# Optimization experiments

Measured on AMD Instinct MI355X. Metric: run time of the kernel, lower is better.

## Reference

```python
import jax, jax.numpy as jnp
import numpy as np

B, S, H, NH = 4, 1024, 768, 12
HD = H // NH  # head dim = 64


def setup_inputs() -> dict:
    key = jax.random.key(0)
    ks = jax.random.split(key, 8)
    scale = 0.02
    return {
        "hidden_states": jax.random.normal(ks[0], (B, S, H), jnp.float32),
        "attention_mask": jax.random.randint(ks[1], (B, 1, 1, S), 0, 2, jnp.int32),
        "rel_pos": jax.random.normal(ks[2], (B, NH, S, S), jnp.float32),
        "rel_2d_pos": jax.random.normal(ks[3], (B, NH, S, S), jnp.float32),
        "Wq": jax.random.normal(ks[4], (H, H), jnp.float32) * scale,
        "bq": jnp.zeros((H,), jnp.float32),
        "Wk": jax.random.normal(ks[5], (H, H), jnp.float32) * scale,
        "bk": jnp.zeros((H,), jnp.float32),
        "Wv": jax.random.normal(ks[6], (H, H), jnp.float32) * scale,
        "bv": jnp.zeros((H,), jnp.float32),
    }


def _heads(x):
    # [B,S,H] -> [B,NH,S,HD]
    return x.reshape(B, S, NH, HD).transpose(0, 2, 1, 3)


def reference(hidden_states, attention_mask, rel_pos, rel_2d_pos, Wq, bq, Wk, bk, Wv, bv):
    q = _heads(hidden_states @ Wq.T + bq) / jnp.sqrt(jnp.asarray(HD, hidden_states.dtype))
    k = _heads(hidden_states @ Wk.T + bk)
    v = _heads(hidden_states @ Wv.T + bv)
    # [B,NH,S,S] scores with additive relative 1D and 2D spatial biases
    scores = jnp.einsum("bhqd,bhkd->bhqk", q, k) + rel_pos + rel_2d_pos
    neg_min = jnp.finfo(jnp.float32).min
    scores = jnp.where(attention_mask.astype(bool), neg_min, scores.astype(jnp.float32))
    probs = jax.nn.softmax(scores, axis=-1).astype(v.dtype)  # dropout p applied only in training
    ctx = jnp.einsum("bhqk,bhkd->bhqd", probs, v)
    return ctx.transpose(0, 2, 1, 3).reshape(B, S, H)
```

## Files before the change

### kernel.cpp

```cpp
#include <hip/hip_runtime.h>
#include <hip/hip_bf16.h>
#include <cstdint>
#include <cstddef>

#define NB 4
#define SEQ 1024
#define HID 768
#define NHEAD 12
#define HD 64

typedef __bf16 bf16x8 __attribute__((ext_vector_type(8)));
typedef float f32x4 __attribute__((ext_vector_type(4)));

__device__ __forceinline__ unsigned short f2bf(float f) {
    unsigned int u = __float_as_uint(f);
    u += 0x7FFFu + ((u >> 16) & 1u);
    return (unsigned short)(u >> 16);
}

__global__ __launch_bounds__(256)
void qkv_kernel(const float* __restrict__ X,
                const float* __restrict__ Wq, const float* __restrict__ bq,
                const float* __restrict__ Wk, const float* __restrict__ bk,
                const float* __restrict__ Wv, const float* __restrict__ bv,
                unsigned short* __restrict__ qws,
                unsigned short* __restrict__ kws,
                unsigned short* __restrict__ vtws)
{
    __shared__ __align__(16) unsigned short Al[128 * 64];
    __shared__ __align__(16) unsigned short Bl[128 * 64];

    const int z = blockIdx.z;
    const float* Wp = (z == 0) ? Wq : ((z == 1) ? Wk : Wv);
    const float* bp = (z == 0) ? bq : ((z == 1) ? bk : bv);
    const int m0 = blockIdx.x * 128;
    const int n0 = blockIdx.y * 128;
    const int t = threadIdx.x;
    const int lane = t & 63;
    const int w = t >> 6;
    const int wm = w >> 1, wn = w & 1;
    const int l15 = lane & 15, l4 = lane >> 4;

    const f32x4 fzero = {0.f, 0.f, 0.f, 0.f};
    f32x4 acc[4][4];
#pragma unroll
    for (int a = 0; a < 4; ++a)
#pragma unroll
        for (int c = 0; c < 4; ++c) acc[a][c] = fzero;

    for (int k0 = 0; k0 < HID; k0 += 64) {
        __syncthreads();
#pragma unroll
        for (int i = 0; i < 8; ++i) {
            int idx = t + 256 * i;
            int row = idx >> 4;
            int c4  = idx & 15;
            float4 va = *(const float4*)(X + (size_t)(m0 + row) * HID + k0 + c4 * 4);
            ushort4 ua = make_ushort4(f2bf(va.x), f2bf(va.y), f2bf(va.z), f2bf(va.w));
            *(ushort4*)(Al + row * 64 + c4 * 4) = ua;
            float4 vb = *(const float4*)(Wp + (size_t)(n0 + row) * HID + k0 + c4 * 4);
            ushort4 ub = make_ushort4(f2bf(vb.x), f2bf(vb.y), f2bf(vb.z), f2bf(vb.w));
            *(ushort4*)(Bl + row * 64 + c4 * 4) = ub;
        }
        __syncthreads();
#pragma unroll
        for (int kc = 0; kc < 2; ++kc) {
            bf16x8 af[4], bfr[4];
#pragma unroll
            for (int mf = 0; mf < 4; ++mf)
                af[mf] = *(const bf16x8*)(Al + (wm * 64 + mf * 16 + l15) * 64 + kc * 32 + l4 * 8);
#pragma unroll
            for (int nf = 0; nf < 4; ++nf)
                bfr[nf] = *(const bf16x8*)(Bl + (wn * 64 + nf * 16 + l15) * 64 + kc * 32 + l4 * 8);
#pragma unroll
            for (int mf = 0; mf < 4; ++mf)
#pragma unroll
                for (int nf = 0; nf < 4; ++nf)
                    acc[mf][nf] = __builtin_amdgcn_mfma_f32_16x16x32_bf16(
                        af[mf], bfr[nf], acc[mf][nf], 0, 0, 0);
        }
    }

#pragma unroll
    for (int nf = 0; nf < 4; ++nf) {
        int n = n0 + wn * 64 + nf * 16 + l15;
        float bias = bp[n];
        int h = n >> 6;
        int d = n & 63;
#pragma unroll
        for (int mf = 0; mf < 4; ++mf) {
            int mbase = m0 + wm * 64 + mf * 16 + l4 * 4;
            int bb = mbase >> 10;
            int srow = mbase & 1023;
            if (z == 2) {
                ushort4 u = make_ushort4(f2bf(acc[mf][nf][0] + bias),
                                         f2bf(acc[mf][nf][1] + bias),
                                         f2bf(acc[mf][nf][2] + bias),
                                         f2bf(acc[mf][nf][3] + bias));
                *(ushort4*)(vtws + ((size_t)(bb * NHEAD + h) * HD + d) * SEQ + srow) = u;
            } else {
                float sc = (z == 0) ? 0.125f : 1.0f;
                unsigned short* dst = (z == 0) ? qws : kws;
#pragma unroll
                for (int j = 0; j < 4; ++j)
                    dst[((size_t)(bb * NHEAD + h) * SEQ + srow + j) * HD + d] =
                        f2bf((acc[mf][nf][j] + bias) * sc);
            }
        }
    }
}

__global__ __launch_bounds__(256)
void attn_kernel(const unsigned short* __restrict__ qws,
                 const unsigned short* __restrict__ kws,
                 const unsigned short* __restrict__ vtws,
                 const float* __restrict__ rel,
                 const float* __restrict__ rel2d,
                 const int* __restrict__ mask,
                 float* __restrict__ out)
{
    __shared__ __align__(16) unsigned short Kl[64 * 64];
    __shared__ __align__(16) unsigned short Vl[64 * 64];
    __shared__ __align__(16) unsigned short Pl[4][16 * 64];

    const int qt = blockIdx.x;
    const int h  = blockIdx.y;
    const int b  = blockIdx.z;
    const int t = threadIdx.x;
    const int lane = t & 63;
    const int w = t >> 6;
    const int l15 = lane & 15, l4 = lane >> 4;

    const size_t headoff = (size_t)(b * NHEAD + h) * SEQ * HD;
    const unsigned short* qh  = qws + headoff;
    const unsigned short* kh  = kws + headoff;
    const unsigned short* vth = vtws + headoff;
    const int q0 = qt * 64 + w * 16;

    bf16x8 qf[2];
#pragma unroll
    for (int kc = 0; kc < 2; ++kc)
        qf[kc] = *(const bf16x8*)(qh + (size_t)(q0 + l15) * HD + kc * 32 + l4 * 8);

    const f32x4 fzero = {0.f, 0.f, 0.f, 0.f};
    float m_run[4], l_run[4];
    f32x4 acc[4];
#pragma unroll
    for (int j = 0; j < 4; ++j) { m_run[j] = -INFINITY; l_run[j] = 0.f; }
#pragma unroll
    for (int df = 0; df < 4; ++df) acc[df] = fzero;

    const float* relh  = rel   + (size_t)(b * NHEAD + h) * SEQ * SEQ;
    const float* rel2h = rel2d + (size_t)(b * NHEAD + h) * SEQ * SEQ;
    const int* maskb = mask + b * SEQ;

    for (int kv0 = 0; kv0 < SEQ; kv0 += 64) {
        __syncthreads();
        {
            const uint4* srcK = (const uint4*)(kh + (size_t)kv0 * HD);
            ((uint4*)Kl)[t]       = srcK[t];
            ((uint4*)Kl)[t + 256] = srcK[t + 256];
            int u0 = t,       r0 = u0 >> 3, s0 = u0 & 7;
            ((uint4*)Vl)[u0] = *(const uint4*)(vth + (size_t)r0 * SEQ + kv0 + s0 * 8);
            int u1 = t + 256, r1 = u1 >> 3, s1 = u1 & 7;
            ((uint4*)Vl)[u1] = *(const uint4*)(vth + (size_t)r1 * SEQ + kv0 + s1 * 8);
        }
        __syncthreads();

        f32x4 sacc[4];
#pragma unroll
        for (int nf = 0; nf < 4; ++nf) sacc[nf] = fzero;
#pragma unroll
        for (int kc = 0; kc < 2; ++kc) {
#pragma unroll
            for (int nf = 0; nf < 4; ++nf) {
                bf16x8 kf = *(const bf16x8*)(Kl + (nf * 16 + l15) * 64 + kc * 32 + l4 * 8);
                sacc[nf] = __builtin_amdgcn_mfma_f32_16x16x32_bf16(qf[kc], kf, sacc[nf], 0, 0, 0);
            }
        }

        float p[4][4];
        float tmax[4] = {-INFINITY, -INFINITY, -INFINITY, -INFINITY};
#pragma unroll
        for (int nf = 0; nf < 4; ++nf) {
            int kcol = kv0 + nf * 16 + l15;
            int mv = maskb[kcol];
            const float* r1p = relh  + (size_t)(q0 + l4 * 4) * SEQ + kcol;
            const float* r2p = rel2h + (size_t)(q0 + l4 * 4) * SEQ + kcol;
#pragma unroll
            for (int j = 0; j < 4; ++j) {
                float sv = sacc[nf][j] + r1p[(size_t)j * SEQ] + r2p[(size_t)j * SEQ];
                sv = mv ? -3.402823466e38f : sv;
                p[nf][j] = sv;
                tmax[j] = fmaxf(tmax[j], sv);
            }
        }
#pragma unroll
        for (int j = 0; j < 4; ++j) {
#pragma unroll
            for (int off = 1; off < 16; off <<= 1)
                tmax[j] = fmaxf(tmax[j], __shfl_xor(tmax[j], off, 64));
        }
        float scal[4], tsum[4];
#pragma unroll
        for (int j = 0; j < 4; ++j) {
            float mnew = fmaxf(m_run[j], tmax[j]);
            scal[j] = __expf(m_run[j] - mnew);
            m_run[j] = mnew;
            tsum[j] = 0.f;
        }
#pragma unroll
        for (int nf = 0; nf < 4; ++nf)
#pragma unroll
            for (int j = 0; j < 4; ++j) {
                p[nf][j] = __expf(p[nf][j] - m_run[j]);
                tsum[j] += p[nf][j];
            }
#pragma unroll
        for (int j = 0; j < 4; ++j) {
#pragma unroll
            for (int off = 1; off < 16; off <<= 1)
                tsum[j] += __shfl_xor(tsum[j], off, 64);
            l_run[j] = l_run[j] * scal[j] + tsum[j];
        }
#pragma unroll
        for (int df = 0; df < 4; ++df)
#pragma unroll
            for (int j = 0; j < 4; ++j)
                acc[df][j] *= scal[j];

        unsigned short* Pw = &Pl[w][0];
#pragma unroll
        for (int nf = 0; nf < 4; ++nf)
#pragma unroll
            for (int j = 0; j < 4; ++j)
                Pw[(l4 * 4 + j) * 64 + nf * 16 + l15] = f2bf(p[nf][j]);
        __syncthreads();

#pragma unroll
        for (int kc = 0; kc < 2; ++kc) {
            bf16x8 pf = *(const bf16x8*)(Pw + l15 * 64 + kc * 32 + l4 * 8);
#pragma unroll
            for (int df = 0; df < 4; ++df) {
                bf16x8 vf = *(const bf16x8*)(Vl + (df * 16 + l15) * 64 + kc * 32 + l4 * 8);
                acc[df] = __builtin_amdgcn_mfma_f32_16x16x32_bf16(pf, vf, acc[df], 0, 0, 0);
            }
        }
    }

#pragma unroll
    for (int df = 0; df < 4; ++df) {
        int d = df * 16 + l15;
#pragma unroll
        for (int j = 0; j < 4; ++j) {
            int qr = q0 + l4 * 4 + j;
            out[((size_t)b * SEQ + qr) * HID + h * HD + d] = acc[df][j] / l_run[j];
        }
    }
}

extern "C" void kernel_launch(void* const* d_in, const int* in_sizes, int n_in,
                              void* d_out, int out_size, void* d_ws, size_t ws_size,
                              hipStream_t stream)
{
    const float* hidden = (const float*)d_in[0];
    const int*   amask  = (const int*)d_in[1];
    const float* rel    = (const float*)d_in[2];
    const float* rel2d  = (const float*)d_in[3];
    const float* Wq = (const float*)d_in[4];
    const float* bq = (const float*)d_in[5];
    const float* Wk = (const float*)d_in[6];
    const float* bk = (const float*)d_in[7];
    const float* Wv = (const float*)d_in[8];
    const float* bv = (const float*)d_in[9];
    float* out = (float*)d_out;

    const size_t per = (size_t)NB * NHEAD * SEQ * HD;
    unsigned short* qws  = (unsigned short*)d_ws;
    unsigned short* kws  = qws + per;
    unsigned short* vtws = kws + per;

    qkv_kernel<<<dim3(32, 6, 3), 256, 0, stream>>>(hidden, Wq, bq, Wk, bk, Wv, bv,
                                                   qws, kws, vtws);
    attn_kernel<<<dim3(16, 12, 4), 256, 0, stream>>>(qws, kws, vtws, rel, rel2d,
                                                     amask, out);
}
```

Measured before the change: 612.5 us.

## Pre-convert inputs to bf16, use direct-to-LDS loads, double-buffer KV, transpose attention MFMA

Adds a separate conversion kernel that writes X and the three weight matrices as bf16, so the QKV GEMM can stage tiles straight into LDS with global_load_lds instead of converting inside every tile. The attention kernel now double-buffers K/V tiles with async LDS loads and an XOR swizzle, and swaps the MFMA operand order so each lane owns one query row. That lets it load the rel bias and mask as vectors, shrink the row reductions to two shuffles, and write float4 outputs. The cost is an extra kernel launch plus extra workspace traffic for the bf16 copies.

Measured after the change: 490.8 us. 1.25x faster.

```diff
diff --git a/kernel.cpp b/kernel.cpp
--- a/kernel.cpp
+++ b/kernel.cpp
@@ -8,9 +8,18 @@
 #define HID 768
 #define NHEAD 12
 #define HD 64
+#define NX (NB * SEQ * HID)
+#define NW (HID * HID)
 
 typedef __bf16 bf16x8 __attribute__((ext_vector_type(8)));
 typedef float f32x4 __attribute__((ext_vector_type(4)));
+
+typedef __attribute__((address_space(3))) void lds_void;
+typedef const __attribute__((address_space(1))) void gbl_void;
+
+__device__ __forceinline__ void gload_lds16(const void* gsrc, void* ldst) {
+    __builtin_amdgcn_global_load_lds((gbl_void*)gsrc, (lds_void*)ldst, 16, 0, 0);
+}
 
 __device__ __forceinline__ unsigned short f2bf(float f) {
     unsigned int u = __float_as_uint(f);
@@ -19,10 +28,35 @@
 }
 
 __global__ __launch_bounds__(256)
-void qkv_kernel(const float* __restrict__ X,
-                const float* __restrict__ Wq, const float* __restrict__ bq,
-                const float* __restrict__ Wk, const float* __restrict__ bk,
-                const float* __restrict__ Wv, const float* __restrict__ bv,
+void convert_kernel(const float* __restrict__ X,
+                    const float* __restrict__ Wq, const float* __restrict__ Wk,
+                    const float* __restrict__ Wv,
+                    unsigned short* __restrict__ Xb,
+                    unsigned short* __restrict__ Wallb)
+{
+    int idx = blockIdx.x * 256 + threadIdx.x;
+    const int NX4 = NX / 4, NW4 = NW / 4;
+    float4 v;
+    unsigned short* dst;
+    if (idx < NX4) {
+        v = ((const float4*)X)[idx];
+        dst = Xb + (size_t)idx * 4;
+    } else {
+        int j = idx - NX4;
+        int z = j / NW4;
+        int r = j - z * NW4;
+        const float* W = (z == 0) ? Wq : ((z == 1) ? Wk : Wv);
+        v = ((const float4*)W)[r];
+        dst = Wallb + (size_t)z * NW + (size_t)r * 4;
+    }
+    *(ushort4*)dst = make_ushort4(f2bf(v.x), f2bf(v.y), f2bf(v.z), f2bf(v.w));
+}
+
+__global__ __launch_bounds__(256)
+void qkv_kernel(const unsigned short* __restrict__ Xb,
+                const unsigned short* __restrict__ Wallb,
+                const float* __restrict__ bq, const float* __restrict__ bk,
+                const float* __restrict__ bv,
                 unsigned short* __restrict__ qws,
                 unsigned short* __restrict__ kws,
                 unsigned short* __restrict__ vtws)
@@ -30,16 +64,15 @@
     __shared__ __align__(16) unsigned short Al[128 * 64];
     __shared__ __align__(16) unsigned short Bl[128 * 64];
 
-    const int z = blockIdx.z;
-    const float* Wp = (z == 0) ? Wq : ((z == 1) ? Wk : Wv);
-    const float* bp = (z == 0) ? bq : ((z == 1) ? bk : bv);
     const int m0 = blockIdx.x * 128;
-    const int n0 = blockIdx.y * 128;
+    const int n0g = blockIdx.y * 128;
     const int t = threadIdx.x;
     const int lane = t & 63;
     const int w = t >> 6;
     const int wm = w >> 1, wn = w & 1;
     const int l15 = lane & 15, l4 = lane >> 4;
+    const int rowA = lane >> 3;
+    const int cEl = (lane & 7) * 8;
 
     const f32x4 fzero = {0.f, 0.f, 0.f, 0.f};
     f32x4 acc[4][4];
@@ -51,16 +84,10 @@
     for (int k0 = 0; k0 < HID; k0 += 64) {
         __syncthreads();
 #pragma unroll
-        for (int i = 0; i < 8; ++i) {
-            int idx = t + 256 * i;
-            int row = idx >> 4;
-            int c4  = idx & 15;
-            float4 va = *(const float4*)(X + (size_t)(m0 + row) * HID + k0 + c4 * 4);
-            ushort4 ua = make_ushort4(f2bf(va.x), f2bf(va.y), f2bf(va.z), f2bf(va.w));
-            *(ushort4*)(Al + row * 64 + c4 * 4) = ua;
-            float4 vb = *(const float4*)(Wp + (size_t)(n0 + row) * HID + k0 + c4 * 4);
-            ushort4 ub = make_ushort4(f2bf(vb.x), f2bf(vb.y), f2bf(vb.z), f2bf(vb.w));
-            *(ushort4*)(Bl + row * 64 + c4 * 4) = ub;
+        for (int i = 0; i < 4; ++i) {
+            int r = w * 32 + i * 8;
+            gload_lds16(Xb + (size_t)(m0 + r + rowA) * HID + k0 + cEl, Al + r * 64);
+            gload_lds16(Wallb + (size_t)(n0g + r + rowA) * HID + k0 + cEl, Bl + r * 64);
         }
         __syncthreads();
 #pragma unroll
@@ -81,9 +108,13 @@
         }
     }
 
+    const int z = n0g / HID;
+    const int nz0 = n0g - z * HID;
+    const float* bp = (z == 0) ? bq : ((z == 1) ? bk : bv);
+
 #pragma unroll
     for (int nf = 0; nf < 4; ++nf) {
-        int n = n0 + wn * 64 + nf * 16 + l15;
+        int n = nz0 + wn * 64 + nf * 16 + l15;
         float bias = bp[n];
         int h = n >> 6;
         int d = n & 63;
@@ -110,6 +141,28 @@
     }
 }
 
+__device__ __forceinline__ void stage_kv(const unsigned short* kh,
+                                         const unsigned short* vth,
+                                         unsigned short* Kd, unsigned short* Vd,
+                                         int kv0, int w, int lane)
+{
+    int r8 = lane >> 3;
+    int swzB = (((lane & 7) ^ r8) * 16);
+#pragma unroll
+    for (int i = 0; i < 2; ++i) {
+        int rb = w * 16 + i * 8;
+        gload_lds16((const char*)(kh + (size_t)(kv0 + rb + r8) * HD) + swzB,
+                    Kd + rb * 64);
+        gload_lds16((const char*)(vth + (size_t)(rb + r8) * SEQ + kv0) + swzB,
+                    Vd + rb * 64);
+    }
+}
+
+__device__ __forceinline__ const bf16x8* swz_rd(const unsigned short* base, int row, int colbyte) {
+    int phys = (row * 128 + colbyte) ^ ((row & 7) << 4);
+    return (const bf16x8*)((const char*)base + phys);
+}
+
 __global__ __launch_bounds__(256)
 void attn_kernel(const unsigned short* __restrict__ qws,
                  const unsigned short* __restrict__ kws,
@@ -119,8 +172,8 @@
                  const int* __restrict__ mask,
                  float* __restrict__ out)
 {
-    __shared__ __align__(16) unsigned short Kl[64 * 64];
-    __shared__ __align__(16) unsigned short Vl[64 * 64];
+    __shared__ __align__(16) unsigned short Kl[2][64 * 64];
+    __shared__ __align__(16) unsigned short Vl[2][64 * 64];
     __shared__ __align__(16) unsigned short Pl[4][16 * 64];
 
     const int qt = blockIdx.x;
@@ -136,37 +189,44 @@
     const unsigned short* kh  = kws + headoff;
     const unsigned short* vth = vtws + headoff;
     const int q0 = qt * 64 + w * 16;
+    const int qrow = q0 + l15;
 
     bf16x8 qf[2];
 #pragma unroll
     for (int kc = 0; kc < 2; ++kc)
-        qf[kc] = *(const bf16x8*)(qh + (size_t)(q0 + l15) * HD + kc * 32 + l4 * 8);
+        qf[kc] = *(const bf16x8*)(qh + (size_t)qrow * HD + kc * 32 + l4 * 8);
 
     const f32x4 fzero = {0.f, 0.f, 0.f, 0.f};
-    float m_run[4], l_run[4];
+    float m_run = -INFINITY, l_run = 0.f;
     f32x4 acc[4];
 #pragma unroll
-    for (int j = 0; j < 4; ++j) { m_run[j] = -INFINITY; l_run[j] = 0.f; }
-#pragma unroll
     for (int df = 0; df < 4; ++df) acc[df] = fzero;
 
-    const float* relh  = rel   + (size_t)(b * NHEAD + h) * SEQ * SEQ;
-    const float* rel2h = rel2d + (size_t)(b * NHEAD + h) * SEQ * SEQ;
-    const int* maskb = mask + b * SEQ;
-
-    for (int kv0 = 0; kv0 < SEQ; kv0 += 64) {
+    const float* r1base = rel   + ((size_t)(b * NHEAD + h) * SEQ + qrow) * SEQ + l4 * 4;
+    const float* r2base = rel2d + ((size_t)(b * NHEAD + h) * SEQ + qrow) * SEQ + l4 * 4;
+    const int* mb4 = mask + b * SEQ + l4 * 4;
+    unsigned short* Pw = Pl[w];
+
+    stage_kv(kh, vth, Kl[0], Vl[0], 0, w, lane);
+    int cur = 0;
+
+    for (int tt = 0; tt < 16; ++tt) {
+        const int kv0 = tt * 64;
         __syncthreads();
-        {
-            const uint4* srcK = (const uint4*)(kh + (size_t)kv0 * HD);
-            ((uint4*)Kl)[t]       = srcK[t];
-            ((uint4*)Kl)[t + 256] = srcK[t + 256];
-            int u0 = t,       r0 = u0 >> 3, s0 = u0 & 7;
-            ((uint4*)Vl)[u0] = *(const uint4*)(vth + (size_t)r0 * SEQ + kv0 + s0 * 8);
-            int u1 = t + 256, r1 = u1 >> 3, s1 = u1 & 7;
-            ((uint4*)Vl)[u1] = *(const uint4*)(vth + (size_t)r1 * SEQ + kv0 + s1 * 8);
-        }
-        __syncthreads();
-
+        if (tt < 15)
+            stage_kv(kh, vth, Kl[cur ^ 1], Vl[cur ^ 1], kv0 + 64, w, lane);
+
+        float4 b1[4], b2[4];
+        int4 mv[4];
+#pragma unroll
+        for (int nf = 0; nf < 4; ++nf) {
+            b1[nf] = *(const float4*)(r1base + kv0 + nf * 16);
+            b2[nf] = *(const float4*)(r2base + kv0 + nf * 16);
+            mv[nf] = *(const int4*)(mb4 + kv0 + nf * 16);
+        }
+
+        const unsigned short* Kc = Kl[cur];
+        const unsigned short* Vc = Vl[cur];
         f32x4 sacc[4];
 #pragma unroll
         for (int nf = 0; nf < 4; ++nf) sacc[nf] = fzero;
@@ -174,88 +234,74 @@
         for (int kc = 0; kc < 2; ++kc) {
 #pragma unroll
             for (int nf = 0; nf < 4; ++nf) {
-                bf16x8 kf = *(const bf16x8*)(Kl + (nf * 16 + l15) * 64 + kc * 32 + l4 * 8);
-                sacc[nf] = __builtin_amdgcn_mfma_f32_16x16x32_bf16(qf[kc], kf, sacc[nf], 0, 0, 0);
-            }
-        }
-
-        float p[4][4];
-        float tmax[4] = {-INFINITY, -INFINITY, -INFINITY, -INFINITY};
+                bf16x8 kf = *swz_rd(Kc, nf * 16 + l15, kc * 64 + l4 * 16);
+                sacc[nf] = __builtin_amdgcn_mfma_f32_16x16x32_bf16(kf, qf[kc], sacc[nf], 0, 0, 0);
+            }
+        }
+
+        float pv[4][4];
+        float tmax = -INFINITY;
 #pragma unroll
         for (int nf = 0; nf < 4; ++nf) {
-            int kcol = kv0 + nf * 16 + l15;
-            int mv = maskb[kcol];
-            const float* r1p = relh  + (size_t)(q0 + l4 * 4) * SEQ + kcol;
-            const float* r2p = rel2h + (size_t)(q0 + l4 * 4) * SEQ + kcol;
+            float bx[4] = {b1[nf].x + b2[nf].x, b1[nf].y + b2[nf].y,
+                           b1[nf].z + b2[nf].z, b1[nf].w + b2[nf].w};
+            int mm[4] = {mv[nf].x, mv[nf].y, mv[nf].z, mv[nf].w};
 #pragma unroll
             for (int j = 0; j < 4; ++j) {
-                float sv = sacc[nf][j] + r1p[(size_t)j * SEQ] + r2p[(size_t)j * SEQ];
-                sv = mv ? -3.402823466e38f : sv;
-                p[nf][j] = sv;
-                tmax[j] = fmaxf(tmax[j], sv);
-            }
-        }
-#pragma unroll
-        for (int j = 0; j < 4; ++j) {
-#pragma unroll
-            for (int off = 1; off < 16; off <<= 1)
-                tmax[j] = fmaxf(tmax[j], __shfl_xor(tmax[j], off, 64));
-        }
-        float scal[4], tsum[4];
-#pragma unroll
-        for (int j = 0; j < 4; ++j) {
-            float mnew = fmaxf(m_run[j], tmax[j]);
-            scal[j] = __expf(m_run[j] - mnew);
-            m_run[j] = mnew;
-            tsum[j] = 0.f;
-        }
+                float sv = mm[j] ? -3.402823466e38f : (sacc[nf][j] + bx[j]);
+                pv[nf][j] = sv;
+                tmax = fmaxf(tmax, sv);
+            }
+        }
+        tmax = fmaxf(tmax, __shfl_xor(tmax, 16, 64));
+        tmax = fmaxf(tmax, __shfl_xor(tmax, 32, 64));
+
+        float mnew = fmaxf(m_run, tmax);
+        float scal = __expf(m_run - mnew);
+        m_run = mnew;
+        float tsum = 0.f;
 #pragma unroll
         for (int nf = 0; nf < 4; ++nf)
 #pragma unroll
             for (int j = 0; j < 4; ++j) {
-                p[nf][j] = __expf(p[nf][j] - m_run[j]);
-                tsum[j] += p[nf][j];
-            }
-#pragma unroll
-        for (int j = 0; j < 4; ++j) {
-#pragma unroll
-            for (int off = 1; off < 16; off <<= 1)
-                tsum[j] += __shfl_xor(tsum[j], off, 64);
-            l_run[j] = l_run[j] * scal[j] + tsum[j];
-        }
+                pv[nf][j] = __expf(pv[nf][j] - mnew);
+                tsum += pv[nf][j];
+            }
+        tsum += __shfl_xor(tsum, 16, 64);
+        tsum += __shfl_xor(tsum, 32, 64);
+        l_run = l_run * scal + tsum;
 #pragma unroll
         for (int df = 0; df < 4; ++df)
 #pragma unroll
-            for (int j = 0; j < 4; ++j)
-                acc[df][j] *= scal[j];
-
-        unsigned short* Pw = &Pl[w][0];
-#pragma unroll
-        for (int nf = 0; nf < 4; ++nf)
-#pragma unroll
-            for (int j = 0; j < 4; ++j)
-                Pw[(l4 * 4 + j) * 64 + nf * 16 + l15] = f2bf(p[nf][j]);
-        __syncthreads();
+            for (int j = 0; j < 4; ++j) acc[df][j] *= scal;
+
+#pragma unroll
+        for (int nf = 0; nf < 4; ++nf) {
+            ushort4 u = make_ushort4(f2bf(pv[nf][0]), f2bf(pv[nf][1]),
+                                     f2bf(pv[nf][2]), f2bf(pv[nf][3]));
+            int linb = l15 * 128 + nf * 32 + l4 * 8;
+            *(ushort4*)((char*)Pw + (linb ^ ((l15 & 7) << 4))) = u;
+        }
 
 #pragma unroll
         for (int kc = 0; kc < 2; ++kc) {
-            bf16x8 pf = *(const bf16x8*)(Pw + l15 * 64 + kc * 32 + l4 * 8);
+            bf16x8 pf = *swz_rd(Pw, l15, kc * 64 + l4 * 16);
 #pragma unroll
             for (int df = 0; df < 4; ++df) {
-                bf16x8 vf = *(const bf16x8*)(Vl + (df * 16 + l15) * 64 + kc * 32 + l4 * 8);
-                acc[df] = __builtin_amdgcn_mfma_f32_16x16x32_bf16(pf, vf, acc[df], 0, 0, 0);
-            }
-        }
-    }
-
+                bf16x8 vf = *swz_rd(Vc, df * 16 + l15, kc * 64 + l4 * 16);
+                acc[df] = __builtin_amdgcn_mfma_f32_16x16x32_bf16(vf, pf, acc[df], 0, 0, 0);
+            }
+        }
+        cur ^= 1;
+    }
+
+    const float inv_l = 1.0f / l_run;
+    float* ob = out + ((size_t)b * SEQ + qrow) * HID + h * HD + l4 * 4;
 #pragma unroll
     for (int df = 0; df < 4; ++df) {
-        int d = df * 16 + l15;
-#pragma unroll
-        for (int j = 0; j < 4; ++j) {
-            int qr = q0 + l4 * 4 + j;
-            out[((size_t)b * SEQ + qr) * HID + h * HD + d] = acc[df][j] / l_run[j];
-        }
+        float4 o = make_float4(acc[df][0] * inv_l, acc[df][1] * inv_l,
+                               acc[df][2] * inv_l, acc[df][3] * inv_l);
+        *(float4*)(ob + df * 16) = o;
     }
 }
 
@@ -276,12 +322,16 @@
     float* out = (float*)d_out;
 
     const size_t per = (size_t)NB * NHEAD * SEQ * HD;
-    unsigned short* qws  = (unsigned short*)d_ws;
-    unsigned short* kws  = qws + per;
-    unsigned short* vtws = kws + per;
-
-    qkv_kernel<<<dim3(32, 6, 3), 256, 0, stream>>>(hidden, Wq, bq, Wk, bk, Wv, bv,
-                                                   qws, kws, vtws);
-    attn_kernel<<<dim3(16, 12, 4), 256, 0, stream>>>(qws, kws, vtws, rel, rel2d,
-                                                     amask, out);
-}
+    unsigned short* qws   = (unsigned short*)d_ws;
+    unsigned short* kws   = qws + per;
+    unsigned short* vtws  = kws + per;
+    unsigned short* Xb    = vtws + per;
+    unsigned short* Wallb = Xb + (size_t)NX;
+
+    convert_kernel<<<dim3((NX + 3 * NW) / 1024), 256, 0, stream>>>(
+        hidden, Wq, Wk, Wv, Xb, Wallb);
+    qkv_kernel<<<dim3(32, 18), 256, 0, stream>>>(Xb, Wallb, bq, bk, bv,
+                                                 qws, kws, vtws);
+    attn_kernel<<<dim3(16, NHEAD, NB), 256, 0, stream>>>(qws, kws, vtws, rel, rel2d,
+                                                         amask, out);
+}
```
